# Performance work log

Hardware: AMD Instinct MI355X
Metric: run time of the kernel (lower is better)

## Reference

```python
import jax, jax.numpy as jnp
import numpy as np
import math

S, B, D, H = 2048, 2, 1024, 16
DK = D // H

def setup_inputs() -> dict:
    key = jax.random.key(0)
    ks = jax.random.split(key, 32)
    f = lambda k, shape, s=1.0: jax.random.normal(k, shape, dtype=jnp.float32) * s
    inp = {
        'qx': f(ks[0], (S, B, D)),
        'kx': f(ks[1], (S, B, D)),
        'vx': f(ks[2], (S, B, D)),
        'qc': f(ks[3], (S, B, D)),
        'kc': f(ks[4], (S, B, D)),
    }
    w = 1.0 / math.sqrt(D)
    names = ['qx_lin', 'kx_lin', 'vx_lin', 'qc_lin', 'kc_lin', 'out_lin']
    for i, n in enumerate(names):
        inp['W_' + n] = f(ks[5 + 2 * i], (D, D), w)
        inp['b_' + n] = f(ks[6 + 2 * i], (D,), w)
    vnames = ['Vqx', 'Vqc', 'Vkx', 'Vkc']
    for i, n in enumerate(vnames):
        inp['W_' + n] = f(ks[17 + 2 * i], (D, 1), w)
        inp['b_' + n] = f(ks[18 + 2 * i], (1,), w)
    return inp

def _forward(qx, kx, vx, qc, kc,
             W_qx_lin, b_qx_lin, W_kx_lin, b_kx_lin, W_vx_lin, b_vx_lin,
             W_qc_lin, b_qc_lin, W_kc_lin, b_kc_lin, W_out_lin, b_out_lin,
             W_Vqx, b_Vqx, W_Vqc, b_Vqc, W_Vkx, b_Vkx, W_Vkc, b_Vkc):
    # [S,B,D] -> [B,S,D]
    qx = jnp.swapaxes(qx, 0, 1)
    kx = jnp.swapaxes(kx, 0, 1)
    vx = jnp.swapaxes(vx, 0, 1)
    qc = jnp.swapaxes(qc, 0, 1)
    kc = jnp.swapaxes(kc, 0, 1)
    bs = qx.shape[0]

    qx = qx @ W_qx_lin + b_qx_lin
    kx = kx @ W_kx_lin + b_kx_lin
    v = vx @ W_vx_lin + b_vx_lin
    qc = qc @ W_qc_lin + b_qc_lin
    kc = kc @ W_kc_lin + b_kc_lin

    lam_q = jax.nn.sigmoid((qx @ W_Vqx + b_Vqx) + (qc @ W_Vqc + b_Vqc))  # [B,S,1]
    lam_k = jax.nn.sigmoid((kx @ W_Vkx + b_Vkx) + (kc @ W_Vkc + b_Vkc))
    q = (1.0 - lam_q) * qx + lam_q * qc
    k = (1.0 - lam_k) * kx + lam_k * kc

    # [B,S,D] -> [B,H,S,dk]
    q = q.reshape(bs, -1, H, DK).transpose(0, 2, 1, 3)
    k = k.reshape(bs, -1, H, DK).transpose(0, 2, 1, 3)
    v = v.reshape(bs, -1, H, DK).transpose(0, 2, 1, 3)

    scores = jnp.einsum('bhqd,bhkd->bhqk', q, k) / math.sqrt(DK)
    attn = jax.nn.softmax(scores, axis=-1)  # dropout is identity in eval
    ctx = jnp.einsum('bhqk,bhkd->bhqd', attn, v)

    concat = ctx.transpose(0, 2, 1, 3).reshape(bs, -1, D)
    out = concat @ W_out_lin + b_out_lin
    return jnp.swapaxes(out, 0, 1)  # back to [S,B,D]

def reference(qx, kx, vx, qc, kc,
              W_qx_lin, b_qx_lin, W_kx_lin, b_kx_lin, W_vx_lin, b_vx_lin,
              W_qc_lin, b_qc_lin, W_kc_lin, b_kc_lin, W_out_lin, b_out_lin,
              W_Vqx, b_Vqx, W_Vqc, b_Vqc, W_Vkx, b_Vkx, W_Vkc, b_Vkc):
    return _forward(qx, kx, vx, qc, kc,
                    W_qx_lin, b_qx_lin, W_kx_lin, b_kx_lin, W_vx_lin, b_vx_lin,
                    W_qc_lin, b_qc_lin, W_kc_lin, b_kc_lin, W_out_lin, b_out_lin,
                    W_Vqx, b_Vqx, W_Vqc, b_Vqc, W_Vkx, b_Vkx, W_Vkc, b_Vkc)
```

## Files before the change

### kernel.cpp

```cpp
#include <hip/hip_runtime.h>
#include <math.h>

typedef unsigned short u16;
typedef __attribute__((ext_vector_type(8))) short short8;
typedef __attribute__((ext_vector_type(4))) float floatx4;
typedef __attribute__((ext_vector_type(4))) unsigned short ushort4v;
typedef __attribute__((ext_vector_type(2))) unsigned int uint2v;

__device__ __forceinline__ float bf2f(u16 x) {
    union { unsigned int u; float f; } v; v.u = ((unsigned int)x) << 16; return v.f;
}
__device__ __forceinline__ u16 f2bf(float f) {
    union { float f; unsigned int u; } v; v.f = f;
    unsigned int r = v.u + 0x7fffu + ((v.u >> 16) & 1u);
    return (u16)(r >> 16);
}
__device__ __forceinline__ unsigned int pk2bf(float a, float b) {
#if __has_builtin(__builtin_amdgcn_cvt_pk_bf16_f32)
    auto r = __builtin_amdgcn_cvt_pk_bf16_f32(a, b);
    union { decltype(r) v; unsigned int u; } cv; cv.v = r; return cv.u;
#else
    return (unsigned int)f2bf(a) | ((unsigned int)f2bf(b) << 16);
#endif
}

__device__ __forceinline__ void gl_lds16(const void* g, void* l) {
    __builtin_amdgcn_global_load_lds(
        (const __attribute__((address_space(1))) unsigned int*)g,
        (__attribute__((address_space(3))) unsigned int*)l,
        16, 0, 0);
}

struct WFuseJobs { const float* W[4]; const float* wv[4]; float* out[4]; };

__global__ __launch_bounds__(256) void wfuse(WFuseJobs wf) {
    const int z = blockIdx.y;
    const float* W = wf.W[z];
    const float* wv = wf.wv[z];
    float* out = wf.out[z];
    const int lane = threadIdx.x & 63, w = threadIdx.x >> 6;
#pragma unroll
    for (int i = 0; i < 4; i++) {
        const int row = blockIdx.x * 16 + w * 4 + i;
        const float* Wr = W + (size_t)row * 1024 + lane * 16;
        const float* vr = wv + lane * 16;
        float p = 0.f;
#pragma unroll
        for (int c = 0; c < 4; c++) {
            const floatx4 a = *(const floatx4*)(Wr + c * 4);
            const floatx4 b = *(const floatx4*)(vr + c * 4);
            p += a[0] * b[0] + a[1] * b[1] + a[2] * b[2] + a[3] * b[3];
        }
#pragma unroll
        for (int m = 1; m <= 32; m <<= 1) p += __shfl_xor(p, m);
        if (lane == 0) out[row] = p;
    }
}

struct CastJobs { const float* src[5]; u16* dst[5]; const float* w[5]; float* dot[5]; };

__global__ __launch_bounds__(256) void castbf(CastJobs cj) {
    const int z = blockIdx.y;
    const int row = blockIdx.x;
    const int t = threadIdx.x;
    const size_t i = (size_t)row * 256 + t;
    const floatx4 v = *(const floatx4*)(cj.src[z] + i * 4);
    ushort4v o;
#pragma unroll
    for (int j = 0; j < 4; j++) o[j] = f2bf(v[j]);
    *(ushort4v*)(cj.dst[z] + i * 4) = o;

    if (cj.w[z]) {
        const floatx4 wv = *(const floatx4*)(cj.w[z] + t * 4);
        float p = v[0] * wv[0] + v[1] * wv[1] + v[2] * wv[2] + v[3] * wv[3];
#pragma unroll
        for (int m = 1; m <= 32; m <<= 1) p += __shfl_xor(p, m);
        __shared__ float red[4];
        if ((t & 63) == 0) red[t >> 6] = p;
        __syncthreads();
        if (t == 0) cj.dot[z][row] = red[0] + red[1] + red[2] + red[3];
    }
}

struct LamJobs {
    const float* dA[2]; const float* dB[2];
    const float* b1[2]; const float* b2[2];
    const float* wv1[2]; const float* wv2[2];
    const float* s1[2]; const float* s2[2];
    float* lam[2];
};

__global__ __launch_bounds__(256) void lamk(LamJobs lj) {
    const int z = blockIdx.y;
    const int t = threadIdx.x;
    float p = 0.f;
    {
        const floatx4 a1 = *(const floatx4*)(lj.b1[z] + t * 4);
        const floatx4 w1 = *(const floatx4*)(lj.wv1[z] + t * 4);
        const floatx4 a2 = *(const floatx4*)(lj.b2[z] + t * 4);
        const floatx4 w2 = *(const floatx4*)(lj.wv2[z] + t * 4);
#pragma unroll
        for (int j = 0; j < 4; j++) p += a1[j] * w1[j] + a2[j] * w2[j];
    }
#pragma unroll
    for (int m = 1; m <= 32; m <<= 1) p += __shfl_xor(p, m);
    __shared__ float red[4];
    if ((t & 63) == 0) red[t >> 6] = p;
    __syncthreads();
    const float c = red[0] + red[1] + red[2] + red[3] + lj.s1[z][0] + lj.s2[z][0];
    const int row = blockIdx.x * 256 + t;
    const float x = lj.dA[z][row] + lj.dB[z][row] + c;
    lj.lam[z][row] = 1.f / (1.f + exp2f(-x * 1.44269504f));
}

struct WTJobs { const float* src[6]; u16* dst[6]; };

__global__ __launch_bounds__(256) void wtrans(WTJobs wj) {
    __shared__ float tile[32][33];
    const int z = blockIdx.z;
    const float* W = wj.src[z];
    u16* Wt = wj.dst[z];
    const int n0 = blockIdx.x * 32, k0 = blockIdx.y * 32;
    const int tx = threadIdx.x & 31, ty = threadIdx.x >> 5;
#pragma unroll
    for (int i = 0; i < 4; i++)
        tile[ty + i * 8][tx] = W[(size_t)(k0 + ty + i * 8) * 1024 + n0 + tx];
    __syncthreads();
#pragma unroll
    for (int i = 0; i < 4; i++)
        Wt[(size_t)(n0 + ty + i * 8) * 1024 + k0 + tx] = f2bf(tile[tx][ty + i * 8]);
}

__global__ __launch_bounds__(256) void vtrans(const u16* __restrict__ V,
                                              u16* __restrict__ Vtg) {
    __shared__ u16 tile[32][34];
    const int bh = blockIdx.z, b = bh >> 4, h = bh & 15;
    const int base = b * 1024 + h * 64;
    const int s0 = blockIdx.x * 32, d0 = blockIdx.y * 32;
    const int tx = threadIdx.x & 31, ty = threadIdx.x >> 5;
#pragma unroll
    for (int i = 0; i < 4; i++)
        tile[ty + i * 8][tx] = V[(size_t)(s0 + ty + i * 8) * 2048 + base + d0 + tx];
    __syncthreads();
#pragma unroll
    for (int i = 0; i < 4; i++)
        Vtg[((size_t)bh * 64 + d0 + ty + i * 8) * 2048 + s0 + tx] = tile[tx][ty + i * 8];
}

struct PJob {
    const u16* Aa; const u16* Ac; const u16* Ba; const u16* Bc;
    const float* biasA; const float* biasC; const float* lam; u16* out;
};
struct PJobs { PJob j[3]; };

__global__ __launch_bounds__(256, 2) void projall(PJobs jobs) {
    __shared__ u16 Asa[128 * 32];
    __shared__ u16 Asc[128 * 32];
    __shared__ u16 Bsa[128 * 32];
    __shared__ u16 Bsc[128 * 32];
    const PJob jb = jobs.j[blockIdx.z];
    const int K = 1024;
    const int m0 = blockIdx.y * 128;
    const int n0 = blockIdx.x * 128;
    const int t = threadIdx.x;
    const int lane = t & 63;
    const int wid = t >> 6;
    const int wm = wid >> 1, wn = wid & 1;
    const int qd = lane >> 4, lm = lane & 15;

    const floatx4 zero4 = {0.f, 0.f, 0.f, 0.f};
    const int e0 = t * 8;
    const int r0 = e0 >> 5, c0 = e0 & 31;
    const int e1 = (256 + t) * 8;
    const int r1 = e1 >> 5, c1 = e1 & 31;

    const u16* Aab = jb.Aa + (size_t)m0 * K;
    const u16* Bab = jb.Ba + (size_t)n0 * K;

    if (jb.Ac) {
        floatx4 accA[4][4], accC[4][4];
#pragma unroll
        for (int i = 0; i < 4; i++)
#pragma unroll
            for (int j2 = 0; j2 < 4; j2++) { accA[i][j2] = zero4; accC[i][j2] = zero4; }
        const u16* Acb = jb.Ac + (size_t)m0 * K;
        const u16* Bcb = jb.Bc + (size_t)n0 * K;

        for (int k0 = 0; k0 < K; k0 += 32) {
            __syncthreads();
            gl_lds16(Aab + (size_t)r0 * K + k0 + c0, &Asa[e0]);
            gl_lds16(Aab + (size_t)r1 * K + k0 + c1, &Asa[e1]);
            gl_lds16(Acb + (size_t)r0 * K + k0 + c0, &Asc[e0]);
            gl_lds16(Acb + (size_t)r1 * K + k0 + c1, &Asc[e1]);
            gl_lds16(Bab + (size_t)r0 * K + k0 + c0, &Bsa[e0]);
            gl_lds16(Bab + (size_t)r1 * K + k0 + c1, &Bsa[e1]);
            gl_lds16(Bcb + (size_t)r0 * K + k0 + c0, &Bsc[e0]);
            gl_lds16(Bcb + (size_t)r1 * K + k0 + c1, &Bsc[e1]);
            __syncthreads();

            short8 aa[4], ac[4], ba[4], bc[4];
#pragma unroll
            for (int i = 0; i < 4; i++) {
                aa[i] = *(const short8*)&Asa[(wm * 64 + i * 16 + lm) * 32 + qd * 8];
                ac[i] = *(const short8*)&Asc[(wm * 64 + i * 16 + lm) * 32 + qd * 8];
                ba[i] = *(const short8*)&Bsa[(wn * 64 + i * 16 + lm) * 32 + qd * 8];
                bc[i] = *(const short8*)&Bsc[(wn * 64 + i * 16 + lm) * 32 + qd * 8];
            }
#pragma unroll
            for (int i = 0; i < 4; i++)
#pragma unroll
                for (int j2 = 0; j2 < 4; j2++) {
                    accA[i][j2] = __builtin_amdgcn_mfma_f32_16x16x32_bf16(aa[i], ba[j2], accA[i][j2], 0, 0, 0);
                    accC[i][j2] = __builtin_amdgcn_mfma_f32_16x16x32_bf16(ac[i], bc[j2], accC[i][j2], 0, 0, 0);
                }
        }

#pragma unroll
        for (int i = 0; i < 4; i++) {
            const int mb = m0 + wm * 64 + i * 16 + qd * 4;
            float lamv[4];
#pragma unroll
            for (int r = 0; r < 4; r++) lamv[r] = jb.lam[mb + r];
#pragma unroll
            for (int j2 = 0; j2 < 4; j2++) {
                const int col = n0 + wn * 64 + j2 * 16 + lm;
                const float bA = jb.biasA[col];
                const float bC = jb.biasC[col];
#pragma unroll
                for (int r = 0; r < 4; r++) {
                    const float va = accA[i][j2][r] + bA;
                    const float vc = accC[i][j2][r] + bC;
                    jb.out[(size_t)(mb + r) * 1024 + col] = f2bf(va + lamv[r] * (vc - va));
                }
            }
        }
    } else {
        floatx4 acc[4][4];
#pragma unroll
        for (int i = 0; i < 4; i++)
#pragma unroll
            for (int j2 = 0; j2 < 4; j2++) acc[i][j2] = zero4;

        for (int k0 = 0; k0 < K; k0 += 32) {
            __syncthreads();
            gl_lds16(Aab + (size_t)r0 * K + k0 + c0, &Asa[e0]);
            gl_lds16(Aab + (size_t)r1 * K + k0 + c1, &Asa[e1]);
            gl_lds16(Bab + (size_t)r0 * K + k0 + c0, &Bsa[e0]);
            gl_lds16(Bab + (size_t)r1 * K + k0 + c1, &Bsa[e1]);
            __syncthreads();

            short8 af[4], bfg[4];
#pragma unroll
            for (int i = 0; i < 4; i++) {
                af[i]  = *(const short8*)&Asa[(wm * 64 + i * 16 + lm) * 32 + qd * 8];
                bfg[i] = *(const short8*)&Bsa[(wn * 64 + i * 16 + lm) * 32 + qd * 8];
            }
#pragma unroll
            for (int i = 0; i < 4; i++)
#pragma unroll
                for (int j2 = 0; j2 < 4; j2++)
                    acc[i][j2] = __builtin_amdgcn_mfma_f32_16x16x32_bf16(af[i], bfg[j2], acc[i][j2], 0, 0, 0);
        }

#pragma unroll
        for (int i = 0; i < 4; i++) {
            const int mb = m0 + wm * 64 + i * 16 + qd * 4;
#pragma unroll
            for (int j2 = 0; j2 < 4; j2++) {
                const int col = n0 + wn * 64 + j2 * 16 + lm;
                const float bv = jb.biasA[col];
#pragma unroll
                for (int r = 0; r < 4; r++)
                    jb.out[(size_t)(mb + r) * 1024 + col] = f2bf(acc[i][j2][r] + bv);
            }
        }
    }
}

__global__ __launch_bounds__(256, 4) void gemm64(const u16* __restrict__ A,
                                                 const u16* __restrict__ Bt,
                                                 const float* __restrict__ bias,
                                                 float* __restrict__ C) {
    __shared__ u16 As[64 * 32];
    __shared__ u16 Bs[128 * 32];
    const int K = 1024;
    const int m0 = blockIdx.y * 64;
    const int n0 = blockIdx.x * 128;
    const int t = threadIdx.x;
    const int lane = t & 63;
    const int wid = t >> 6;
    const int wm = wid >> 1, wn = wid & 1;
    const int qd = lane >> 4, lm = lane & 15;

    const floatx4 zero4 = {0.f, 0.f, 0.f, 0.f};
    floatx4 acc[2][4];
#pragma unroll
    for (int i = 0; i < 2; i++)
#pragma unroll
        for (int j2 = 0; j2 < 4; j2++) acc[i][j2] = zero4;

    const u16* Ab = A + (size_t)m0 * K;
    const u16* Bb = Bt + (size_t)n0 * K;
    const int e0 = t * 8;
    const int r0 = e0 >> 5, c0 = e0 & 31;
    const int e1 = (256 + t) * 8;
    const int r1 = e1 >> 5, c1 = e1 & 31;

    for (int k0 = 0; k0 < K; k0 += 32) {
        __syncthreads();
        gl_lds16(Ab + (size_t)r0 * K + k0 + c0, &As[e0]);
        gl_lds16(Bb + (size_t)r0 * K + k0 + c0, &Bs[e0]);
        gl_lds16(Bb + (size_t)r1 * K + k0 + c1, &Bs[e1]);
        __syncthreads();

        short8 af[2], bfg[4];
#pragma unroll
        for (int i = 0; i < 2; i++)
            af[i] = *(const short8*)&As[(wm * 32 + i * 16 + lm) * 32 + qd * 8];
#pragma unroll
        for (int j2 = 0; j2 < 4; j2++)
            bfg[j2] = *(const short8*)&Bs[(wn * 64 + j2 * 16 + lm) * 32 + qd * 8];
#pragma unroll
        for (int i = 0; i < 2; i++)
#pragma unroll
            for (int j2 = 0; j2 < 4; j2++)
                acc[i][j2] = __builtin_amdgcn_mfma_f32_16x16x32_bf16(af[i], bfg[j2], acc[i][j2], 0, 0, 0);
    }

#pragma unroll
    for (int i = 0; i < 2; i++) {
        const int mb = m0 + wm * 32 + i * 16 + qd * 4;
#pragma unroll
        for (int j2 = 0; j2 < 4; j2++) {
            const int col = n0 + wn * 64 + j2 * 16 + lm;
            const float bv = bias[col];
#pragma unroll
            for (int r = 0; r < 4; r++)
                C[(size_t)(mb + r) * 1024 + col] = acc[i][j2][r] + bv;
        }
    }
}

__global__ __launch_bounds__(256, 2) void attn4(
    const u16* __restrict__ Q, const u16* __restrict__ Kk,
    const u16* __restrict__ Vtg, float* __restrict__ ctxp,
    float* __restrict__ lp) {
    __shared__ u16 Ks[64 * 72];
    __shared__ u16 Vs[64 * 72];
    __shared__ u16 Ps[4 * 64 * 72];

    const int bh = blockIdx.y, b = bh >> 4, h = bh & 15;
    const int sp = blockIdx.z;
    const int base = b * 1024 + h * 64;
    const int t = threadIdx.x, lane = t & 63, w = t >> 6;
    const int qd = lane >> 4, lm = lane & 15;
    const int q0w = blockIdx.x * 256 + w * 64;

    short8 qf[4][2];
#pragma unroll
    for (int qh = 0; qh < 4; qh++) {
        const u16* qr = Q + (size_t)(q0w + qh * 16 + lm) * 2048 + base;
#pragma unroll
        for (int c = 0; c < 2; c++)
            qf[qh][c] = *(const short8*)(qr + c * 32 + qd * 8);
    }

    const floatx4 zero4 = {0.f, 0.f, 0.f, 0.f};
    floatx4 ctx[4][4];
#pragma unroll
    for (int qh = 0; qh < 4; qh++)
#pragma unroll
        for (int g = 0; g < 4; g++) ctx[qh][g] = zero4;
    float lpart[4] = {0.f, 0.f, 0.f, 0.f};

    u16* Pw = &Ps[w * 64 * 72];
    const float C = 0.18033688011112042f;

    const int sr = t >> 3, sc = (t & 7) * 8;
    const u16* ksrc = Kk + (size_t)(sp * 1024 + sr) * 2048 + base + sc;
    const u16* vsrc = Vtg + ((size_t)bh * 64 + sr) * 2048 + sp * 1024 + sc;
    u16* kdst0 = &Ks[sr * 72 + sc];
    u16* kdst1 = &Ks[(sr + 32) * 72 + sc];
    u16* vdst0 = &Vs[sr * 72 + sc];
    u16* vdst1 = &Vs[(sr + 32) * 72 + sc];

    short8 ka0 = *(const short8*)ksrc;
    short8 ka1 = *(const short8*)(ksrc + (size_t)32 * 2048);
    short8 va0 = *(const short8*)vsrc;
    short8 va1 = *(const short8*)(vsrc + (size_t)32 * 2048);

    for (int kt = 0; kt < 16; kt++) {
        __syncthreads();
        *(short8*)kdst0 = ka0;
        *(short8*)kdst1 = ka1;
        *(short8*)vdst0 = va0;
        *(short8*)vdst1 = va1;
        __syncthreads();
        if (kt < 15) {
            ksrc += (size_t)64 * 2048;
            vsrc += 64;
            ka0 = *(const short8*)ksrc;
            ka1 = *(const short8*)(ksrc + (size_t)32 * 2048);
            va0 = *(const short8*)vsrc;
            va1 = *(const short8*)(vsrc + (size_t)32 * 2048);
        }

#pragma unroll
        for (int g = 0; g < 4; g++) {
            const short8 kf0 = *(const short8*)&Ks[(g * 16 + lm) * 72 + qd * 8];
            const short8 kf1 = *(const short8*)&Ks[(g * 16 + lm) * 72 + 32 + qd * 8];
#pragma unroll
            for (int qh = 0; qh < 4; qh++) {
                floatx4 st = zero4;
                st = __builtin_amdgcn_mfma_f32_16x16x32_bf16(kf0, qf[qh][0], st, 0, 0, 0);
                st = __builtin_amdgcn_mfma_f32_16x16x32_bf16(kf1, qf[qh][1], st, 0, 0, 0);
                const float p0 = exp2f(st[0] * C);
                const float p1 = exp2f(st[1] * C);
                const float p2 = exp2f(st[2] * C);
                const float p3 = exp2f(st[3] * C);
                lpart[qh] += (p0 + p1) + (p2 + p3);
                uint2v pw;
                pw[0] = pk2bf(p0, p1);
                pw[1] = pk2bf(p2, p3);
                *(uint2v*)&Pw[(qh * 16 + lm) * 72 + g * 16 + qd * 4] = pw;
            }
        }

        short8 pa[4][2];
#pragma unroll
        for (int qh = 0; qh < 4; qh++)
#pragma unroll
            for (int c = 0; c < 2; c++)
                pa[qh][c] = *(const short8*)&Pw[(qh * 16 + lm) * 72 + c * 32 + qd * 8];
#pragma unroll
        for (int g = 0; g < 4; g++) {
            const short8 vb0 = *(const short8*)&Vs[(g * 16 + lm) * 72 + qd * 8];
            const short8 vb1 = *(const short8*)&Vs[(g * 16 + lm) * 72 + 32 + qd * 8];
#pragma unroll
            for (int qh = 0; qh < 4; qh++) {
                ctx[qh][g] = __builtin_amdgcn_mfma_f32_16x16x32_bf16(pa[qh][0], vb0, ctx[qh][g], 0, 0, 0);
                ctx[qh][g] = __builtin_amdgcn_mfma_f32_16x16x32_bf16(pa[qh][1], vb1, ctx[qh][g], 0, 0, 0);
            }
        }
    }

    float* cbase = ctxp + (size_t)sp * 4194304;
#pragma unroll
    for (int qh = 0; qh < 4; qh++) {
        float l = lpart[qh];
        l += __shfl_xor(l, 16);
        l += __shfl_xor(l, 32);
        if (lane < 16)
            lp[(size_t)sp * 65536 + bh * 2048 + q0w + qh * 16 + lane] = l;
#pragma unroll
        for (int r = 0; r < 4; r++) {
            const int srow = q0w + qh * 16 + qd * 4 + r;
            float* orow = cbase + (size_t)srow * 2048 + base;
#pragma unroll
            for (int g = 0; g < 4; g++)
                orow[g * 16 + lm] = ctx[qh][g][r];
        }
    }
}

__global__ __launch_bounds__(256) void merge(const float* __restrict__ ctxp,
                                             const float* __restrict__ lp,
                                             u16* __restrict__ out) {
    const size_t idx = ((size_t)blockIdx.x * 256 + threadIdx.x) * 4;
    const floatx4 a = *(const floatx4*)(ctxp + idx);
    const floatx4 c = *(const floatx4*)(ctxp + 4194304 + idx);
    const int srow = (int)(idx >> 11);
    const int rem = (int)(idx & 2047);
    const int bh = rem >> 6;
    const float l = lp[bh * 2048 + srow] + lp[65536 + bh * 2048 + srow];
    const float inv = 1.0f / l;
    ushort4v o;
    const unsigned int lo = pk2bf((a[0] + c[0]) * inv, (a[1] + c[1]) * inv);
    const unsigned int hi = pk2bf((a[2] + c[2]) * inv, (a[3] + c[3]) * inv);
    o[0] = (u16)(lo & 0xffff); o[1] = (u16)(lo >> 16);
    o[2] = (u16)(hi & 0xffff); o[3] = (u16)(hi >> 16);
    *(ushort4v*)(out + idx) = o;
}

extern "C" void kernel_launch(void* const* d_in, const int* in_sizes, int n_in,
                              void* d_out, int out_size, void* d_ws, size_t ws_size,
                              hipStream_t stream) {
    const float* qx = (const float*)d_in[0];
    const float* kx = (const float*)d_in[1];
    const float* vx = (const float*)d_in[2];
    const float* qc = (const float*)d_in[3];
    const float* kc = (const float*)d_in[4];
    const float* W_qx = (const float*)d_in[5];   const float* b_qx = (const float*)d_in[6];
    const float* W_kx = (const float*)d_in[7];   const float* b_kx = (const float*)d_in[8];
    const float* W_vx = (const float*)d_in[9];   const float* b_vx = (const float*)d_in[10];
    const float* W_qc = (const float*)d_in[11];  const float* b_qc = (const float*)d_in[12];
    const float* W_kc = (const float*)d_in[13];  const float* b_kc = (const float*)d_in[14];
    const float* W_out = (const float*)d_in[15]; const float* b_out = (const float*)d_in[16];
    const float* W_Vqx = (const float*)d_in[17]; const float* b_Vqx = (const float*)d_in[18];
    const float* W_Vqc = (const float*)d_in[19]; const float* b_Vqc = (const float*)d_in[20];
    const float* W_Vkx = (const float*)d_in[21]; const float* b_Vkx = (const float*)d_in[22];
    const float* W_Vkc = (const float*)d_in[23]; const float* b_Vkc = (const float*)d_in[24];

    char* ws = (char*)d_ws;
    const size_t NT = 4194304;
    const size_t MB = 1048576;
    u16* Xb[5];
    for (int i = 0; i < 5; i++) Xb[i] = (u16*)(ws + (size_t)i * NT * 2);
    u16* Wt[6];
    for (int i = 0; i < 6; i++) Wt[i] = (u16*)(ws + 40 * MB + (size_t)i * 2 * MB);
    u16* Pv    = (u16*)(ws + 52 * MB);
    u16* qg    = (u16*)(ws + 60 * MB);
    u16* kg    = (u16*)(ws + 68 * MB);
    u16* ctxbf = (u16*)(ws + 76 * MB);
    float* wfused = (float*)(ws + 84 * MB);
    float* dots   = (float*)(ws + 84 * MB + 16384);
    float* lam    = (float*)(ws + 84 * MB + 16384 + 65536);
    float* l_part = (float*)(ws + 84 * MB + 16384 + 65536 + 32768);
    float* ctxp = (float*)ws;
    u16* Vtg    = (u16*)(ws + 32 * MB);

    WFuseJobs wf;
    wf.W[0] = W_qx; wf.wv[0] = W_Vqx; wf.out[0] = wfused;
    wf.W[1] = W_qc; wf.wv[1] = W_Vqc; wf.out[1] = wfused + 1024;
    wf.W[2] = W_kx; wf.wv[2] = W_Vkx; wf.out[2] = wfused + 2048;
    wf.W[3] = W_kc; wf.wv[3] = W_Vkc; wf.out[3] = wfused + 3072;
    wfuse<<<dim3(64, 4), 256, 0, stream>>>(wf);

    CastJobs cj;
    const float* srcs[5] = {qx, kx, vx, qc, kc};
    for (int i = 0; i < 5; i++) { cj.src[i] = srcs[i]; cj.dst[i] = Xb[i]; cj.w[i] = nullptr; cj.dot[i] = nullptr; }
    cj.w[0] = wfused;        cj.dot[0] = dots;
    cj.w[3] = wfused + 1024; cj.dot[3] = dots + 4096;
    cj.w[1] = wfused + 2048; cj.dot[1] = dots + 8192;
    cj.w[4] = wfused + 3072; cj.dot[4] = dots + 12288;
    castbf<<<dim3(4096, 5), 256, 0, stream>>>(cj);

    LamJobs lj;
    lj.dA[0] = dots;        lj.dB[0] = dots + 4096;
    lj.b1[0] = b_qx; lj.b2[0] = b_qc; lj.wv1[0] = W_Vqx; lj.wv2[0] = W_Vqc;
    lj.s1[0] = b_Vqx; lj.s2[0] = b_Vqc; lj.lam[0] = lam;
    lj.dA[1] = dots + 8192; lj.dB[1] = dots + 12288;
    lj.b1[1] = b_kx; lj.b2[1] = b_kc; lj.wv1[1] = W_Vkx; lj.wv2[1] = W_Vkc;
    lj.s1[1] = b_Vkx; lj.s2[1] = b_Vkc; lj.lam[1] = lam + 4096;
    lamk<<<dim3(16, 2), 256, 0, stream>>>(lj);

    WTJobs wj;
    const float* wsrc[6] = {W_qx, W_kx, W_vx, W_qc, W_kc, W_out};
    for (int i = 0; i < 6; i++) { wj.src[i] = wsrc[i]; wj.dst[i] = Wt[i]; }
    wtrans<<<dim3(32, 32, 6), 256, 0, stream>>>(wj);

    PJobs pj;
    pj.j[0].Aa = Xb[0]; pj.j[0].Ac = Xb[3]; pj.j[0].Ba = Wt[0]; pj.j[0].Bc = Wt[3];
    pj.j[0].biasA = b_qx; pj.j[0].biasC = b_qc; pj.j[0].lam = lam;        pj.j[0].out = qg;
    pj.j[1].Aa = Xb[1]; pj.j[1].Ac = Xb[4]; pj.j[1].Ba = Wt[1]; pj.j[1].Bc = Wt[4];
    pj.j[1].biasA = b_kx; pj.j[1].biasC = b_kc; pj.j[1].lam = lam + 4096; pj.j[1].out = kg;
    pj.j[2].Aa = Xb[2]; pj.j[2].Ac = nullptr; pj.j[2].Ba = Wt[2]; pj.j[2].Bc = nullptr;
    pj.j[2].biasA = b_vx; pj.j[2].biasC = nullptr; pj.j[2].lam = nullptr; pj.j[2].out = Pv;
    projall<<<dim3(8, 32, 3), 256, 0, stream>>>(pj);

    vtrans<<<dim3(64, 2, 32), 256, 0, stream>>>(Pv, Vtg);

    attn4<<<dim3(8, 32, 2), 256, 0, stream>>>(qg, kg, Vtg, ctxp, l_part);

    merge<<<4096, 256, 0, stream>>>(ctxp, l_part, ctxbf);

    gemm64<<<dim3(8, 64), 256, 0, stream>>>(ctxbf, Wt[5], b_out, (float*)d_out);
}
```

Measured before the change: 366.8 us.

## Fuse fp32-to-bf16 input cast into projection GEMM with register-prefetched loads

Drops the separate cast kernel that wrote bf16 copies of all five inputs. The projection GEMM now reads fp32 activations directly, converts them to bf16 in registers and stores them to LDS, with the next K-tile prefetched into registers. The lambda gate becomes a per-row dot-product kernel over the fp32 inputs, with the bias-dot term precomputed in wfuse. All GEMMs move from direct global-to-LDS async loads to register-staged loads, which removes a large write-then-reread of activations at the cost of twice the A-side global traffic inside the GEMM and more register pressure.

After: 380.5 us. +3.7%, slower.

```diff
diff --git a/kernel.cpp b/kernel.cpp
--- a/kernel.cpp
+++ b/kernel.cpp
@@ -23,22 +23,23 @@
     return (unsigned int)f2bf(a) | ((unsigned int)f2bf(b) << 16);
 #endif
 }
-
-__device__ __forceinline__ void gl_lds16(const void* g, void* l) {
-    __builtin_amdgcn_global_load_lds(
-        (const __attribute__((address_space(1))) unsigned int*)g,
-        (__attribute__((address_space(3))) unsigned int*)l,
-        16, 0, 0);
-}
-
-struct WFuseJobs { const float* W[4]; const float* wv[4]; float* out[4]; };
+__device__ __forceinline__ short8 cvt8(const floatx4 a, const floatx4 b) {
+    union { unsigned int u[4]; short8 s; } r;
+    r.u[0] = pk2bf(a[0], a[1]); r.u[1] = pk2bf(a[2], a[3]);
+    r.u[2] = pk2bf(b[0], b[1]); r.u[3] = pk2bf(b[2], b[3]);
+    return r.s;
+}
+
+struct WFuseJobs { const float* W[4]; const float* wv[4]; const float* bl[4];
+                   float* out[4]; float* bdot; };
 
 __global__ __launch_bounds__(256) void wfuse(WFuseJobs wf) {
     const int z = blockIdx.y;
     const float* W = wf.W[z];
     const float* wv = wf.wv[z];
     float* out = wf.out[z];
-    const int lane = threadIdx.x & 63, w = threadIdx.x >> 6;
+    const int t = threadIdx.x;
+    const int lane = t & 63, w = t >> 6;
 #pragma unroll
     for (int i = 0; i < 4; i++) {
         const int row = blockIdx.x * 16 + w * 4 + i;
@@ -55,62 +56,50 @@
         for (int m = 1; m <= 32; m <<= 1) p += __shfl_xor(p, m);
         if (lane == 0) out[row] = p;
     }
-}
-
-struct CastJobs { const float* src[5]; u16* dst[5]; const float* w[5]; float* dot[5]; };
-
-__global__ __launch_bounds__(256) void castbf(CastJobs cj) {
-    const int z = blockIdx.y;
-    const int row = blockIdx.x;
-    const int t = threadIdx.x;
-    const size_t i = (size_t)row * 256 + t;
-    const floatx4 v = *(const floatx4*)(cj.src[z] + i * 4);
-    ushort4v o;
-#pragma unroll
-    for (int j = 0; j < 4; j++) o[j] = f2bf(v[j]);
-    *(ushort4v*)(cj.dst[z] + i * 4) = o;
-
-    if (cj.w[z]) {
-        const floatx4 wv = *(const floatx4*)(cj.w[z] + t * 4);
-        float p = v[0] * wv[0] + v[1] * wv[1] + v[2] * wv[2] + v[3] * wv[3];
+    if (blockIdx.x == 0) {
+        const floatx4 bb = *(const floatx4*)(wf.bl[z] + t * 4);
+        const floatx4 vv = *(const floatx4*)(wv + t * 4);
+        float p = bb[0] * vv[0] + bb[1] * vv[1] + bb[2] * vv[2] + bb[3] * vv[3];
 #pragma unroll
         for (int m = 1; m <= 32; m <<= 1) p += __shfl_xor(p, m);
         __shared__ float red[4];
         if ((t & 63) == 0) red[t >> 6] = p;
         __syncthreads();
-        if (t == 0) cj.dot[z][row] = red[0] + red[1] + red[2] + red[3];
-    }
-}
-
-struct LamJobs {
-    const float* dA[2]; const float* dB[2];
-    const float* b1[2]; const float* b2[2];
-    const float* wv1[2]; const float* wv2[2];
-    const float* s1[2]; const float* s2[2];
+        if (t == 0) wf.bdot[z] = red[0] + red[1] + red[2] + red[3];
+    }
+}
+
+struct DotJobs {
+    const float* xa[2]; const float* xc[2];
+    const float* w1[2]; const float* w2[2];
+    const float* bdot;
+    const float* sA[2]; const float* sB[2];
     float* lam[2];
 };
 
-__global__ __launch_bounds__(256) void lamk(LamJobs lj) {
+__global__ __launch_bounds__(256) void dotk(DotJobs dj) {
     const int z = blockIdx.y;
+    const int row = blockIdx.x;
     const int t = threadIdx.x;
+    const size_t off = (size_t)row * 1024 + t * 4;
+    const floatx4 a  = *(const floatx4*)(dj.xa[z] + off);
+    const floatx4 c  = *(const floatx4*)(dj.xc[z] + off);
+    const floatx4 w1 = *(const floatx4*)(dj.w1[z] + t * 4);
+    const floatx4 w2 = *(const floatx4*)(dj.w2[z] + t * 4);
     float p = 0.f;
-    {
-        const floatx4 a1 = *(const floatx4*)(lj.b1[z] + t * 4);
-        const floatx4 w1 = *(const floatx4*)(lj.wv1[z] + t * 4);
-        const floatx4 a2 = *(const floatx4*)(lj.b2[z] + t * 4);
-        const floatx4 w2 = *(const floatx4*)(lj.wv2[z] + t * 4);
-#pragma unroll
-        for (int j = 0; j < 4; j++) p += a1[j] * w1[j] + a2[j] * w2[j];
-    }
+#pragma unroll
+    for (int j = 0; j < 4; j++) p += a[j] * w1[j] + c[j] * w2[j];
 #pragma unroll
     for (int m = 1; m <= 32; m <<= 1) p += __shfl_xor(p, m);
     __shared__ float red[4];
     if ((t & 63) == 0) red[t >> 6] = p;
     __syncthreads();
-    const float c = red[0] + red[1] + red[2] + red[3] + lj.s1[z][0] + lj.s2[z][0];
-    const int row = blockIdx.x * 256 + t;
-    const float x = lj.dA[z][row] + lj.dB[z][row] + c;
-    lj.lam[z][row] = 1.f / (1.f + exp2f(-x * 1.44269504f));
+    if (t == 0) {
+        const float x = red[0] + red[1] + red[2] + red[3]
+                      + dj.bdot[2 * z] + dj.bdot[2 * z + 1]
+                      + dj.sA[z][0] + dj.sB[z][0];
+        dj.lam[z][row] = 1.f / (1.f + exp2f(-x * 1.44269504f));
+    }
 }
 
 struct WTJobs { const float* src[6]; u16* dst[6]; };
@@ -148,7 +137,7 @@
 }
 
 struct PJob {
-    const u16* Aa; const u16* Ac; const u16* Ba; const u16* Bc;
+    const float* Aa; const float* Ac; const u16* Ba; const u16* Bc;
     const float* biasA; const float* biasC; const float* lam; u16* out;
 };
 struct PJobs { PJob j[3]; };
@@ -168,14 +157,15 @@
     const int wm = wid >> 1, wn = wid & 1;
     const int qd = lane >> 4, lm = lane & 15;
 
+    const int srow = t >> 1, colb = (t & 1) * 16;
+    const float* Aap = jb.Aa + (size_t)(m0 + srow) * K + colb;
+    const u16*   Bap = jb.Ba + (size_t)(n0 + srow) * K + colb;
+    u16* awr  = &Asa[srow * 32 + colb];
+    u16* cwr  = &Asc[srow * 32 + colb];
+    u16* bawr = &Bsa[srow * 32 + colb];
+    u16* bcwr = &Bsc[srow * 32 + colb];
+
     const floatx4 zero4 = {0.f, 0.f, 0.f, 0.f};
-    const int e0 = t * 8;
-    const int r0 = e0 >> 5, c0 = e0 & 31;
-    const int e1 = (256 + t) * 8;
-    const int r1 = e1 >> 5, c1 = e1 & 31;
-
-    const u16* Aab = jb.Aa + (size_t)m0 * K;
-    const u16* Bab = jb.Ba + (size_t)n0 * K;
 
     if (jb.Ac) {
         floatx4 accA[4][4], accC[4][4];
@@ -183,19 +173,33 @@
         for (int i = 0; i < 4; i++)
 #pragma unroll
             for (int j2 = 0; j2 < 4; j2++) { accA[i][j2] = zero4; accC[i][j2] = zero4; }
-        const u16* Acb = jb.Ac + (size_t)m0 * K;
-        const u16* Bcb = jb.Bc + (size_t)n0 * K;
+        const float* Acp = jb.Ac + (size_t)(m0 + srow) * K + colb;
+        const u16*   Bcp = jb.Bc + (size_t)(n0 + srow) * K + colb;
+
+        floatx4 pa[4], pc[4];
+        short8 pba[2], pbc[2];
+#pragma unroll
+        for (int q = 0; q < 4; q++) { pa[q] = *(const floatx4*)(Aap + q * 4); pc[q] = *(const floatx4*)(Acp + q * 4); }
+        pba[0] = *(const short8*)Bap; pba[1] = *(const short8*)(Bap + 8);
+        pbc[0] = *(const short8*)Bcp; pbc[1] = *(const short8*)(Bcp + 8);
 
         for (int k0 = 0; k0 < K; k0 += 32) {
             __syncthreads();
-            gl_lds16(Aab + (size_t)r0 * K + k0 + c0, &Asa[e0]);
-            gl_lds16(Aab + (size_t)r1 * K + k0 + c1, &Asa[e1]);
-            gl_lds16(Acb + (size_t)r0 * K + k0 + c0, &Asc[e0]);
-            gl_lds16(Acb + (size_t)r1 * K + k0 + c1, &Asc[e1]);
-            gl_lds16(Bab + (size_t)r0 * K + k0 + c0, &Bsa[e0]);
-            gl_lds16(Bab + (size_t)r1 * K + k0 + c1, &Bsa[e1]);
-            gl_lds16(Bcb + (size_t)r0 * K + k0 + c0, &Bsc[e0]);
-            gl_lds16(Bcb + (size_t)r1 * K + k0 + c1, &Bsc[e1]);
+            *(short8*)awr        = cvt8(pa[0], pa[1]);
+            *(short8*)(awr + 8)  = cvt8(pa[2], pa[3]);
+            *(short8*)cwr        = cvt8(pc[0], pc[1]);
+            *(short8*)(cwr + 8)  = cvt8(pc[2], pc[3]);
+            *(short8*)bawr       = pba[0];
+            *(short8*)(bawr + 8) = pba[1];
+            *(short8*)bcwr       = pbc[0];
+            *(short8*)(bcwr + 8) = pbc[1];
+            if (k0 + 32 < K) {
+                Aap += 32; Acp += 32; Bap += 32; Bcp += 32;
+#pragma unroll
+                for (int q = 0; q < 4; q++) { pa[q] = *(const floatx4*)(Aap + q * 4); pc[q] = *(const floatx4*)(Acp + q * 4); }
+                pba[0] = *(const short8*)Bap; pba[1] = *(const short8*)(Bap + 8);
+                pbc[0] = *(const short8*)Bcp; pbc[1] = *(const short8*)(Bcp + 8);
+            }
             __syncthreads();
 
             short8 aa[4], ac[4], ba[4], bc[4];
@@ -241,12 +245,24 @@
 #pragma unroll
             for (int j2 = 0; j2 < 4; j2++) acc[i][j2] = zero4;
 
+        floatx4 pa[4];
+        short8 pba[2];
+#pragma unroll
+        for (int q = 0; q < 4; q++) pa[q] = *(const floatx4*)(Aap + q * 4);
+        pba[0] = *(const short8*)Bap; pba[1] = *(const short8*)(Bap + 8);
+
         for (int k0 = 0; k0 < K; k0 += 32) {
             __syncthreads();
-            gl_lds16(Aab + (size_t)r0 * K + k0 + c0, &Asa[e0]);
-            gl_lds16(Aab + (size_t)r1 * K + k0 + c1, &Asa[e1]);
-            gl_lds16(Bab + (size_t)r0 * K + k0 + c0, &Bsa[e0]);
-            gl_lds16(Bab + (size_t)r1 * K + k0 + c1, &Bsa[e1]);
+            *(short8*)awr        = cvt8(pa[0], pa[1]);
+            *(short8*)(awr + 8)  = cvt8(pa[2], pa[3]);
+            *(short8*)bawr       = pba[0];
+            *(short8*)(bawr + 8) = pba[1];
+            if (k0 + 32 < K) {
+                Aap += 32; Bap += 32;
+#pragma unroll
+                for (int q = 0; q < 4; q++) pa[q] = *(const floatx4*)(Aap + q * 4);
+                pba[0] = *(const short8*)Bap; pba[1] = *(const short8*)(Bap + 8);
+            }
             __syncthreads();
 
             short8 af[4], bfg[4];
@@ -299,18 +315,27 @@
 #pragma unroll
         for (int j2 = 0; j2 < 4; j2++) acc[i][j2] = zero4;
 
-    const u16* Ab = A + (size_t)m0 * K;
-    const u16* Bb = Bt + (size_t)n0 * K;
-    const int e0 = t * 8;
-    const int r0 = e0 >> 5, c0 = e0 & 31;
-    const int e1 = (256 + t) * 8;
-    const int r1 = e1 >> 5, c1 = e1 & 31;
+    const int ar = t >> 2, ac_ = (t & 3) * 8;
+    const int br = t >> 1, bc_ = (t & 1) * 16;
+    const u16* Ap = A + (size_t)(m0 + ar) * K + ac_;
+    const u16* Bp = Bt + (size_t)(n0 + br) * K + bc_;
+    u16* awr = &As[ar * 32 + ac_];
+    u16* bwr = &Bs[br * 32 + bc_];
+
+    short8 pa0, pb0, pb1;
+    pa0 = *(const short8*)Ap;
+    pb0 = *(const short8*)Bp; pb1 = *(const short8*)(Bp + 8);
 
     for (int k0 = 0; k0 < K; k0 += 32) {
         __syncthreads();
-        gl_lds16(Ab + (size_t)r0 * K + k0 + c0, &As[e0]);
-        gl_lds16(Bb + (size_t)r0 * K + k0 + c0, &Bs[e0]);
-        gl_lds16(Bb + (size_t)r1 * K + k0 + c1, &Bs[e1]);
+        *(short8*)awr = pa0;
+        *(short8*)bwr = pb0;
+        *(short8*)(bwr + 8) = pb1;
+        if (k0 + 32 < K) {
+            Ap += 32; Bp += 32;
+            pa0 = *(const short8*)Ap;
+            pb0 = *(const short8*)Bp; pb1 = *(const short8*)(Bp + 8);
+        }
         __syncthreads();
 
         short8 af[2], bfg[4];
@@ -502,10 +527,9 @@
     const float* W_Vkc = (const float*)d_in[23]; const float* b_Vkc = (const float*)d_in[24];
 
     char* ws = (char*)d_ws;
-    const size_t NT = 4194304;
     const size_t MB = 1048576;
-    u16* Xb[5];
-    for (int i = 0; i < 5; i++) Xb[i] = (u16*)(ws + (size_t)i * NT * 2);
+    float* ctxp = (float*)ws;
+    u16* Vtg    = (u16*)(ws + 32 * MB);
     u16* Wt[6];
     for (int i = 0; i < 6; i++) Wt[i] = (u16*)(ws + 40 * MB + (size_t)i * 2 * MB);
     u16* Pv    = (u16*)(ws + 52 * MB);
@@ -513,36 +537,25 @@
     u16* kg    = (u16*)(ws + 68 * MB);
     u16* ctxbf = (u16*)(ws + 76 * MB);
     float* wfused = (float*)(ws + 84 * MB);
-    float* dots   = (float*)(ws + 84 * MB + 16384);
-    float* lam    = (float*)(ws + 84 * MB + 16384 + 65536);
-    float* l_part = (float*)(ws + 84 * MB + 16384 + 65536 + 32768);
-    float* ctxp = (float*)ws;
-    u16* Vtg    = (u16*)(ws + 32 * MB);
+    float* bdot   = (float*)(ws + 84 * MB + 16384);
+    float* lam    = (float*)(ws + 84 * MB + 16384 + 256);
+    float* l_part = (float*)(ws + 84 * MB + 16384 + 256 + 32768);
 
     WFuseJobs wf;
-    wf.W[0] = W_qx; wf.wv[0] = W_Vqx; wf.out[0] = wfused;
-    wf.W[1] = W_qc; wf.wv[1] = W_Vqc; wf.out[1] = wfused + 1024;
-    wf.W[2] = W_kx; wf.wv[2] = W_Vkx; wf.out[2] = wfused + 2048;
-    wf.W[3] = W_kc; wf.wv[3] = W_Vkc; wf.out[3] = wfused + 3072;
+    wf.W[0] = W_qx; wf.wv[0] = W_Vqx; wf.bl[0] = b_qx; wf.out[0] = wfused;
+    wf.W[1] = W_qc; wf.wv[1] = W_Vqc; wf.bl[1] = b_qc; wf.out[1] = wfused + 1024;
+    wf.W[2] = W_kx; wf.wv[2] = W_Vkx; wf.bl[2] = b_kx; wf.out[2] = wfused + 2048;
+    wf.W[3] = W_kc; wf.wv[3] = W_Vkc; wf.bl[3] = b_kc; wf.out[3] = wfused + 3072;
+    wf.bdot = bdot;
     wfuse<<<dim3(64, 4), 256, 0, stream>>>(wf);
 
-    CastJobs cj;
-    const float* srcs[5] = {qx, kx, vx, qc, kc};
-    for (int i = 0; i < 5; i++) { cj.src[i] = srcs[i]; cj.dst[i] = Xb[i]; cj.w[i] = nullptr; cj.dot[i] = nullptr; }
-    cj.w[0] = wfused;        cj.dot[0] = dots;
-    cj.w[3] = wfused + 1024; cj.dot[3] = dots + 4096;
-    cj.w[1] = wfused + 2048; cj.dot[1] = dots + 8192;
-    cj.w[4] = wfused + 3072; cj.dot[4] = dots + 12288;
-    castbf<<<dim3(4096, 5), 256, 0, stream>>>(cj);
-
-    LamJobs lj;
-    lj.dA[0] = dots;        lj.dB[0] = dots + 4096;
-    lj.b1[0] = b_qx; lj.b2[0] = b_qc; lj.wv1[0] = W_Vqx; lj.wv2[0] = W_Vqc;
-    lj.s1[0] = b_Vqx; lj.s2[0] = b_Vqc; lj.lam[0] = lam;
-    lj.dA[1] = dots + 8192; lj.dB[1] = dots + 12288;
-    lj.b1[1] = b_kx; lj.b2[1] = b_kc; lj.wv1[1] = W_Vkx; lj.wv2[1] = W_Vkc;
-    lj.s1[1] = b_Vkx; lj.s2[1] = b_Vkc; lj.lam[1] = lam + 4096;
-    lamk<<<dim3(16, 2), 256, 0, stream>>>(lj);
+    DotJobs dj;
+    dj.xa[0] = qx; dj.xc[0] = qc; dj.w1[0] = wfused;        dj.w2[0] = wfused + 1024;
+    dj.sA[0] = b_Vqx; dj.sB[0] = b_Vqc; dj.lam[0] = lam;
+    dj.xa[1] = kx; dj.xc[1] = kc; dj.w1[1] = wfused + 2048; dj.w2[1] = wfused + 3072;
+    dj.sA[1] = b_Vkx; dj.sB[1] = b_Vkc; dj.lam[1] = lam + 4096;
+    dj.bdot = bdot;
+    dotk<<<dim3(4096, 2), 256, 0, stream>>>(dj);
 
     WTJobs wj;
     const float* wsrc[6] = {W_qx, W_kx, W_vx, W_qc, W_kc, W_out};
@@ -550,11 +563,11 @@
     wtrans<<<dim3(32, 32, 6), 256, 0, stream>>>(wj);
 
     PJobs pj;
-    pj.j[0].Aa = Xb[0]; pj.j[0].Ac = Xb[3]; pj.j[0].Ba = Wt[0]; pj.j[0].Bc = Wt[3];
+    pj.j[0].Aa = qx; pj.j[0].Ac = qc; pj.j[0].Ba = Wt[0]; pj.j[0].Bc = Wt[3];
     pj.j[0].biasA = b_qx; pj.j[0].biasC = b_qc; pj.j[0].lam = lam;        pj.j[0].out = qg;
-    pj.j[1].Aa = Xb[1]; pj.j[1].Ac = Xb[4]; pj.j[1].Ba = Wt[1]; pj.j[1].Bc = Wt[4];
+    pj.j[1].Aa = kx; pj.j[1].Ac = kc; pj.j[1].Ba = Wt[1]; pj.j[1].Bc = Wt[4];
     pj.j[1].biasA = b_kx; pj.j[1].biasC = b_kc; pj.j[1].lam = lam + 4096; pj.j[1].out = kg;
-    pj.j[2].Aa = Xb[2]; pj.j[2].Ac = nullptr; pj.j[2].Ba = Wt[2]; pj.j[2].Bc = nullptr;
+    pj.j[2].Aa = vx; pj.j[2].Ac = nullptr; pj.j[2].Ba = Wt[2]; pj.j[2].Bc = nullptr;
     pj.j[2].biasA = b_vx; pj.j[2].biasC = nullptr; pj.j[2].lam = nullptr; pj.j[2].out = Pv;
     projall<<<dim3(8, 32, 3), 256, 0, stream>>>(pj);
 
```
